# Kernel tuning notes

Hardware: AMD Instinct MI355X
Metric: run time of the kernel (lower is better)

The kernel has to match this reference:

```python
import math
import jax, jax.numpy as jnp
import numpy as np

D_MODEL = 1024
N_HEADS = 16
HEAD_DIM = D_MODEL // N_HEADS
ROPE_THETA = 10000.0


def setup_inputs() -> dict:
    key = jax.random.key(0)
    ks = jax.random.split(key, 5)
    B, T = 4, 2048
    # xavier-ish scale for weights
    w_scale = math.sqrt(2.0 / (D_MODEL + D_MODEL))
    return {
        "x": jax.random.normal(ks[0], (B, T, D_MODEL), dtype=jnp.float32),
        "Wq": jax.random.normal(ks[1], (D_MODEL, D_MODEL), dtype=jnp.float32) * w_scale,
        "Wk": jax.random.normal(ks[2], (D_MODEL, D_MODEL), dtype=jnp.float32) * w_scale,
        "Wv": jax.random.normal(ks[3], (D_MODEL, D_MODEL), dtype=jnp.float32) * w_scale,
        "Wo": jax.random.normal(ks[4], (D_MODEL, D_MODEL), dtype=jnp.float32) * w_scale,
    }


def _apply_rope(t, offset=0):
    # t: (B, H, T, Dh); standard half-rotation RoPE
    B, H, T, Dh = t.shape
    inv_freq = 1.0 / (ROPE_THETA ** (jnp.arange(0, Dh, 2, dtype=jnp.float32) / Dh))
    pos = jnp.arange(T, dtype=jnp.float32) + offset  # (T,)
    ang = pos[:, None] * inv_freq[None, :]           # (T, Dh/2)
    cos = jnp.concatenate([jnp.cos(ang), jnp.cos(ang)], axis=-1)  # (T, Dh)
    sin = jnp.concatenate([jnp.sin(ang), jnp.sin(ang)], axis=-1)
    t1, t2 = t[..., : Dh // 2], t[..., Dh // 2 :]
    rot = jnp.concatenate([-t2, t1], axis=-1)
    return t * cos + rot * sin


def _forward(x, Wq, Wk, Wv, Wo):
    B, T, _ = x.shape
    scale = 1.0 / math.sqrt(HEAD_DIM)

    def split_heads(y):  # (B,T,D) -> (B,H,T,Dh)
        return y.reshape(B, T, N_HEADS, HEAD_DIM).transpose(0, 2, 1, 3)

    q = split_heads(x @ Wq.T)
    k = split_heads(x @ Wk.T)
    v = split_heads(x @ Wv.T)

    q = _apply_rope(q)
    k = _apply_rope(k)

    # full materialized scores, as in the original manual SDPA
    scores = jnp.einsum("bhtd,bhsd->bhts", q, k) * scale  # (B,H,T,T)
    causal = jnp.triu(jnp.ones((T, T), dtype=bool), k=1)   # True = masked
    scores = jnp.where(causal[None, None], -jnp.inf, scores)
    attn = jax.nn.softmax(scores, axis=-1)
    attn = jnp.nan_to_num(attn, nan=0.0)
    out = jnp.einsum("bhts,bhsd->bhtd", attn, v)           # (B,H,T,Dh)
    out = out.transpose(0, 2, 1, 3).reshape(B, T, N_HEADS * HEAD_DIM)
    return out @ Wo.T


def reference(x, Wq, Wk, Wv, Wo):
    return _forward(x, Wq, Wk, Wv, Wo)
```

## Files before the change

kernel.cpp:

```cpp
#include <hip/hip_runtime.h>
#include <math.h>

typedef __bf16 bf16_t;
typedef __bf16 bf16x4 __attribute__((ext_vector_type(4)));
typedef __bf16 bf16x8 __attribute__((ext_vector_type(8)));
typedef float f32x4 __attribute__((ext_vector_type(4)));

#define MFMA16(a, b, c) __builtin_amdgcn_mfma_f32_16x16x32_bf16(a, b, c, 0, 0, 0)
#define GLD_LDS16(g, l)                                                                    \
    __builtin_amdgcn_global_load_lds((const __attribute__((address_space(1))) void*)(g),   \
                                     (__attribute__((address_space(3))) void*)(l), 16, 0, 0)

#define SM_SCALE_LOG2E 0.18033688011112042f
#define NEG_LOG2_10K_32 -0.41524101186092029f

#define SWZ(r, u) ((((r) << 6) + (u)) ^ ((((r) >> 1) & 7) << 4))

__device__ __forceinline__ void fast_sincos(float ang, float* s, float* c) {
    float rev = ang * 0.15915494309189535f;
    rev = rev - floorf(rev);
    *s = __builtin_amdgcn_sinf(rev);
    *c = __builtin_amdgcn_cosf(rev);
}

__global__ void cvt_all(const float* __restrict__ x, const float* __restrict__ wq,
                        const float* __restrict__ wk, const float* __restrict__ wv,
                        const float* __restrict__ wo, bf16_t* __restrict__ out) {
    long i = ((long)blockIdx.x * 256 + threadIdx.x) * 4;
    const float* src;
    long off;
    const long M1 = 1048576;
    if (i < 8 * M1) { src = x;  off = i; }
    else if (i < 9 * M1)  { src = wq; off = i - 8 * M1; }
    else if (i < 10 * M1) { src = wk; off = i - 9 * M1; }
    else if (i < 11 * M1) { src = wv; off = i - 10 * M1; }
    else                  { src = wo; off = i - 11 * M1; }
    float4 v = *(const float4*)(src + off);
    bf16x4 pk;
    pk[0] = (bf16_t)v.x;
    pk[1] = (bf16_t)v.y;
    pk[2] = (bf16_t)v.z;
    pk[3] = (bf16_t)v.w;
    *(bf16x4*)(out + i) = pk;
}

template <typename OutT>
__global__ __launch_bounds__(256) void gemm_bt(const bf16_t* __restrict__ A,
                                               const bf16_t* __restrict__ B,
                                               OutT* __restrict__ C,
                                               int M, int N, int K) {
    __shared__ __align__(16) bf16_t As[128 * 32];
    __shared__ __align__(16) bf16_t Bs[128 * 32];
    const int tid = threadIdx.x;
    const int lane = tid & 63, wave = tid >> 6;
    const int qd = lane >> 4, ln = lane & 15;
    int mt = blockIdx.y, nt = blockIdx.x;
    if ((gridDim.y & 7) == 0) {
        const int flat = blockIdx.x + gridDim.x * blockIdx.y;
        const int xcd = flat & 7, idx = flat >> 3;
        const int gy8 = gridDim.y >> 3;
        mt = xcd * gy8 + (idx % gy8);
        nt = idx / gy8;
    }
    const int m0 = mt * 128, n0 = nt * 128;
    const int wr = (wave >> 1) * 64, wc = (wave & 1) * 64;
    const int Kb = K * 2;

    f32x4 acc[4][4];
#pragma unroll
    for (int i = 0; i < 4; ++i)
#pragma unroll
        for (int j = 0; j < 4; ++j)
#pragma unroll
            for (int r = 0; r < 4; ++r) acc[i][j][r] = 0.f;

    const int off0 = wave * 2048 + lane * 16;
    const int off1 = off0 + 1024;
    const int r0 = off0 >> 6, c0 = off0 & 63;
    const int r1 = off1 >> 6, c1 = off1 & 63;

    for (int kt = 0; kt < K; kt += 32) {
        const char* Ab = (const char*)A + (size_t)m0 * Kb + kt * 2;
        const char* Bb = (const char*)B + (size_t)n0 * Kb + kt * 2;
        GLD_LDS16(Ab + (size_t)r0 * Kb + c0, (char*)As + wave * 2048);
        GLD_LDS16(Ab + (size_t)r1 * Kb + c1, (char*)As + wave * 2048 + 1024);
        GLD_LDS16(Bb + (size_t)r0 * Kb + c0, (char*)Bs + wave * 2048);
        GLD_LDS16(Bb + (size_t)r1 * Kb + c1, (char*)Bs + wave * 2048 + 1024);
        __syncthreads();
        bf16x8 af[4], bfr[4];
#pragma unroll
        for (int i = 0; i < 4; ++i)
            af[i] = *(const bf16x8*)(As + (wr + i * 16 + ln) * 32 + qd * 8);
#pragma unroll
        for (int j = 0; j < 4; ++j)
            bfr[j] = *(const bf16x8*)(Bs + (wc + j * 16 + ln) * 32 + qd * 8);
#pragma unroll
        for (int i = 0; i < 4; ++i)
#pragma unroll
            for (int j = 0; j < 4; ++j)
                acc[i][j] = MFMA16(af[i], bfr[j], acc[i][j]);
        __syncthreads();
    }
#pragma unroll
    for (int i = 0; i < 4; ++i)
#pragma unroll
        for (int j = 0; j < 4; ++j)
#pragma unroll
            for (int r = 0; r < 4; ++r) {
                int row = m0 + wr + i * 16 + qd * 4 + r;
                int col = n0 + wc + j * 16 + ln;
                C[(size_t)row * N + col] = (OutT)acc[i][j][r];
            }
}

__global__ __launch_bounds__(256) void gemm_qkv_rope8(const bf16_t* __restrict__ A,
                                                      const bf16_t* __restrict__ B,
                                                      bf16_t* __restrict__ Qo,
                                                      bf16_t* __restrict__ Ko,
                                                      bf16_t* __restrict__ Vt) {
    __shared__ __align__(16) bf16_t LA[2][2][128 * 32];
    __shared__ __align__(16) bf16_t LB[2][2][128 * 32];
    const int tid = threadIdx.x;
    const int wave = tid >> 6, lane = tid & 63;
    const int qd = lane >> 4, ln = lane & 15;
    const int wrr = wave >> 1, wcc = wave & 1;
    const int m0 = blockIdx.y * 128, n0 = blockIdx.x * 128;

    f32x4 acc[4][4];
#pragma unroll
    for (int m = 0; m < 4; ++m)
#pragma unroll
        for (int n = 0; n < 4; ++n)
#pragma unroll
            for (int r = 0; r < 4; ++r) acc[m][n][r] = 0.f;

    const int soff = wave * 1024 + lane * 16;
    const int slog = soff ^ (((soff >> 7) & 7) << 4);
    const int srow = slog >> 6;
    const int scol = slog & 63;
    const char* Abase = (const char*)A + (size_t)(m0 + srow) * 2048 + scol;
    const char* Bbase = (const char*)B + (size_t)(n0 + srow) * 2048 + scol;

    int aoff[4], boff[4];
#pragma unroll
    for (int m = 0; m < 4; ++m) {
        int r = wrr * 64 + m * 16 + ln;
        aoff[m] = ((r << 6) + (qd << 4)) ^ (((r >> 1) & 7) << 4);
    }
#pragma unroll
    for (int n = 0; n < 4; ++n) {
        int r = wcc * 64 + n * 16 + ln;
        boff[n] = ((r << 6) + (qd << 4)) ^ (((r >> 1) & 7) << 4);
    }

    auto stageA = [&](int kt, int kh, int nb) {
        const char* g = Abase + kt * 128 + kh * 64;
        char* l = (char*)&LA[nb][kh][0] + wave * 1024;
        GLD_LDS16(g, l);
        GLD_LDS16(g + (size_t)64 * 2048, l + 4096);
    };
    auto stageB = [&](int kt, int kh, int nb) {
        const char* g = Bbase + kt * 128 + kh * 64;
        char* l = (char*)&LB[nb][kh][0] + wave * 1024;
        GLD_LDS16(g, l);
        GLD_LDS16(g + (size_t)64 * 2048, l + 4096);
    };

    bf16x8 fA[4], fB[4];
#define LOAD_B(kh, bb_)                                          \
    {                                                            \
        const char* base_ = (const char*)&LB[bb_][kh][0];        \
        fB[0] = *(const bf16x8*)(base_ + boff[0]);               \
        fB[1] = *(const bf16x8*)(base_ + boff[1]);               \
        fB[2] = *(const bf16x8*)(base_ + boff[2]);               \
        fB[3] = *(const bf16x8*)(base_ + boff[3]);               \
    }
#define LOAD_A(kh, bb_)                                          \
    {                                                            \
        const char* base_ = (const char*)&LA[bb_][kh][0];        \
        fA[0] = *(const bf16x8*)(base_ + aoff[0]);               \
        fA[1] = *(const bf16x8*)(base_ + aoff[1]);               \
        fA[2] = *(const bf16x8*)(base_ + aoff[2]);               \
        fA[3] = *(const bf16x8*)(base_ + aoff[3]);               \
    }
#define MFMA_Q()                                                                 \
    {                                                                            \
        __builtin_amdgcn_s_setprio(1);                                           \
        _Pragma("unroll") for (int mm = 0; mm < 4; ++mm)                         \
            _Pragma("unroll") for (int nn = 0; nn < 4; ++nn)                     \
                acc[mm][nn] = MFMA16(fA[mm], fB[nn], acc[mm][nn]);               \
        __builtin_amdgcn_s_setprio(0);                                           \
    }
#define BAR __builtin_amdgcn_s_barrier()
#define WAIT_LGKM asm volatile("s_waitcnt lgkmcnt(0)" ::: "memory")
#define VMCNT4 asm volatile("s_waitcnt vmcnt(4)" ::: "memory")
#define VMCNT0 asm volatile("s_waitcnt vmcnt(0)" ::: "memory")

    stageB(0, 0, 0);
    stageA(0, 0, 0);
    stageB(0, 1, 0);
    stageA(0, 1, 0);
    VMCNT4;
    BAR;

    int buf = 0;
    for (int kt = 0; kt < 16; ++kt) {
        const int nb = buf ^ 1;
        const bool pre = (kt + 1 < 16);
        LOAD_B(0, buf);
        LOAD_A(0, buf);
        if (pre) { stageB(kt + 1, 0, nb); stageA(kt + 1, 0, nb); }
        BAR;
        WAIT_LGKM;
        MFMA_Q();
        if (pre) { VMCNT4; } else { VMCNT0; }
        BAR;
        LOAD_B(1, buf);
        LOAD_A(1, buf);
        if (pre) { stageB(kt + 1, 1, nb); stageA(kt + 1, 1, nb); }
        BAR;
        WAIT_LGKM;
        MFMA_Q();
        if (pre) { VMCNT4; } else { VMCNT0; }
        BAR;
        buf = nb;
    }
#undef LOAD_B
#undef LOAD_A
#undef MFMA_Q
#undef BAR
#undef WAIT_LGKM
#undef VMCNT4
#undef VMCNT0

    if (n0 < 2048) {
        const bool isQ = (n0 < 1024);
        bf16_t* Out = isQ ? Qo : Ko;
        const float scale = isQ ? SM_SCALE_LOG2E : 1.0f;
        const int nc0 = (n0 & 1023) + wcc * 64;
        const float inv0 = exp2f((float)ln * NEG_LOG2_10K_32);
        const float inv1 = exp2f((float)(ln + 16) * NEG_LOG2_10K_32);
#pragma unroll
        for (int m = 0; m < 4; ++m) {
#pragma unroll
            for (int r = 0; r < 4; ++r) {
                int row = m0 + wrr * 64 + m * 16 + qd * 4 + r;
                int t = row & 2047, bb = row >> 11;
                float ft = (float)t;
                float s0, c0v, s1, c1v;
                fast_sincos(ft * inv0, &s0, &c0v);
                fast_sincos(ft * inv1, &s1, &c1v);
#pragma unroll
                for (int n = 0; n < 4; ++n) {
                    int col = nc0 + n * 16 + ln;
                    int h = col >> 6, d = col & 63;
                    float sv = (n & 1) ? s1 : s0;
                    float cv = (n & 1) ? c1v : c0v;
                    float td = acc[m][n][r], tp = acc[m][n ^ 2][r];
                    float o = (n < 2) ? (td * cv - tp * sv) : (td * cv + tp * sv);
                    Out[((size_t)(bb * 16 + h) * 2048 + t) * 64 + d] = (bf16_t)(o * scale);
                }
            }
        }
    } else {
        const int nv0 = (n0 - 2048) + wcc * 64;
#pragma unroll
        for (int m = 0; m < 4; ++m) {
            int tb = m0 + wrr * 64 + m * 16 + qd * 4;
            int t = tb & 2047, bb = tb >> 11;
#pragma unroll
            for (int n = 0; n < 4; ++n) {
                int col = nv0 + n * 16 + ln;
                int h = col >> 6, d = col & 63;
                bf16x4 pk;
#pragma unroll
                for (int r = 0; r < 4; ++r) pk[r] = (bf16_t)acc[m][n][r];
                *(bf16x4*)(Vt + ((size_t)(bb * 16 + h) * 64 + d) * 2048 + t) = pk;
            }
        }
    }
}

__global__ __launch_bounds__(256) void attn_fwd(const bf16_t* __restrict__ Qg,
                                                const bf16_t* __restrict__ Kg,
                                                const bf16_t* __restrict__ Vtg,
                                                bf16_t* __restrict__ Og) {
    __shared__ __align__(16) bf16_t Kt[2 * 64 * 32];
    __shared__ __align__(16) bf16_t Vl[2 * 64 * 32];
    __shared__ __align__(16) bf16_t Pl[4][2 * 32 * 32];
    const int id = blockIdx.x;
    const int bh = ((id & 7) << 3) | ((id >> 3) & 7);
    const int pair = (id >> 6) & 7;
    const int b = bh >> 4, h = bh & 15;
    const int tid = threadIdx.x, wave = tid >> 6, lane = tid & 63;
    const int qd = lane >> 4, ln = lane & 15;
    const int kr0r = tid >> 3, kr1r = 32 + (tid >> 3);
    const int ch = tid & 7;
    const int kr0c = ch * 8;
    const int wh = (ch >> 2) * 4096;
    const int wu = (ch & 3) << 4;
    const int wo0 = wh + SWZ(kr0r, wu);
    const int wo1 = wh + SWZ(kr1r, wu);
    const bf16_t* Kbh = Kg + (size_t)bh * 2048 * 64;
    const bf16_t* Vbh = Vtg + (size_t)bh * 64 * 2048;

    bf16x8 vones;
#pragma unroll
    for (int i = 0; i < 8; ++i) vones[i] = (bf16_t)1.0f;

    for (int ph = 0; ph < 2; ++ph) {
        const int qt = ph ? 15 - pair : pair;
        const int q0 = qt * 128;
        const int wrow = q0 + wave * 32;
        const int njt = 2 * qt + 2;

        bf16x8 aq[2][2];
#pragma unroll
        for (int f = 0; f < 2; ++f) {
            const bf16_t* Qbase = Qg + ((size_t)bh * 2048 + wrow + f * 16 + ln) * 64;
            aq[f][0] = *(const bf16x8*)(Qbase + qd * 8);
            aq[f][1] = *(const bf16x8*)(Qbase + 32 + qd * 8);
        }

        f32x4 lsum[2];
        f32x4 o_acc[2][4];
#pragma unroll
        for (int f = 0; f < 2; ++f) {
#pragma unroll
            for (int r = 0; r < 4; ++r) lsum[f][r] = 0.f;
#pragma unroll
            for (int c = 0; c < 4; ++c)
#pragma unroll
                for (int r = 0; r < 4; ++r) o_acc[f][c][r] = 0.f;
        }

        int4 kr0, kr1, vr0, vr1;
        auto issue = [&](int j) {
            const bf16_t* kp = Kbh + (size_t)j * 64 * 64;
            const bf16_t* vp = Vbh + j * 64;
            kr0 = *(const int4*)(kp + kr0r * 64 + kr0c);
            kr1 = *(const int4*)(kp + kr1r * 64 + kr0c);
            vr0 = *(const int4*)(vp + (size_t)kr0r * 2048 + kr0c);
            vr1 = *(const int4*)(vp + (size_t)kr1r * 2048 + kr0c);
        };
        issue(0);

        for (int j = 0; j < njt; ++j) {
            __syncthreads();
            *(int4*)((char*)Kt + wo0) = kr0;
            *(int4*)((char*)Kt + wo1) = kr1;
            *(int4*)((char*)Vl + wo0) = vr0;
            *(int4*)((char*)Vl + wo1) = vr1;
            __syncthreads();
            if (j + 1 < njt) issue(j + 1);

            if (j * 64 > wrow + 31) continue;
            const int j64 = j * 64;

            f32x4 s[2][4];
            __builtin_amdgcn_s_setprio(1);
#pragma unroll
            for (int st = 0; st < 4; ++st) {
                const int rk = st * 16 + ln;
                bf16x8 bk0 = *(const bf16x8*)((const char*)Kt + SWZ(rk, qd * 16));
                bf16x8 bk1 = *(const bf16x8*)((const char*)Kt + 4096 + SWZ(rk, qd * 16));
#pragma unroll
                for (int f = 0; f < 2; ++f) {
                    f32x4 t = {0.f, 0.f, 0.f, 0.f};
                    t = MFMA16(aq[f][0], bk0, t);
                    t = MFMA16(aq[f][1], bk1, t);
                    s[f][st] = t;
                }
            }
            __builtin_amdgcn_s_setprio(0);

            if (j64 + 63 <= wrow) {
#pragma unroll
                for (int f = 0; f < 2; ++f)
#pragma unroll
                    for (int st = 0; st < 4; ++st)
#pragma unroll
                        for (int r = 0; r < 4; ++r)
                            s[f][st][r] = __builtin_amdgcn_exp2f(s[f][st][r]);
            } else {
#pragma unroll
                for (int f = 0; f < 2; ++f) {
                    int rowb = wrow + f * 16 + qd * 4;
#pragma unroll
                    for (int st = 0; st < 4; ++st) {
                        int col = j64 + st * 16 + ln;
#pragma unroll
                        for (int r = 0; r < 4; ++r) {
                            float v = (col > rowb + r) ? -INFINITY : s[f][st][r];
                            s[f][st][r] = __builtin_amdgcn_exp2f(v);
                        }
                    }
                }
            }

            char* Pw = (char*)&Pl[wave][0];
#pragma unroll
            for (int f = 0; f < 2; ++f)
#pragma unroll
                for (int st = 0; st < 4; ++st) {
                    const int ph2 = (st >> 1) * 2048;
                    const int pu = ((st & 1) * 16 + ln) * 2;
#pragma unroll
                    for (int r = 0; r < 4; ++r) {
                        const int prow = f * 16 + qd * 4 + r;
                        *(bf16_t*)(Pw + ph2 + SWZ(prow, pu)) = (bf16_t)s[f][st][r];
                    }
                }

            bf16x8 bv[4][2];
#pragma unroll
            for (int ct = 0; ct < 4; ++ct) {
                const int rv = ct * 16 + ln;
                bv[ct][0] = *(const bf16x8*)((const char*)Vl + SWZ(rv, qd * 16));
                bv[ct][1] = *(const bf16x8*)((const char*)Vl + 4096 + SWZ(rv, qd * 16));
            }
            __builtin_amdgcn_s_setprio(1);
#pragma unroll
            for (int f = 0; f < 2; ++f) {
                const int rp = f * 16 + ln;
                bf16x8 ap0 = *(const bf16x8*)(Pw + SWZ(rp, qd * 16));
                bf16x8 ap1 = *(const bf16x8*)(Pw + 2048 + SWZ(rp, qd * 16));
                lsum[f] = MFMA16(ap0, vones, lsum[f]);
                lsum[f] = MFMA16(ap1, vones, lsum[f]);
#pragma unroll
                for (int ct = 0; ct < 4; ++ct) {
                    o_acc[f][ct] = MFMA16(ap0, bv[ct][0], o_acc[f][ct]);
                    o_acc[f][ct] = MFMA16(ap1, bv[ct][1], o_acc[f][ct]);
                }
            }
            __builtin_amdgcn_s_setprio(0);
        }

#pragma unroll
        for (int f = 0; f < 2; ++f) {
            size_t obase = ((size_t)b * 2048 + wrow + f * 16 + qd * 4) * 1024 + h * 64;
            float rl[4];
#pragma unroll
            for (int r = 0; r < 4; ++r) rl[r] = __builtin_amdgcn_rcpf(lsum[f][r]);
#pragma unroll
            for (int ct = 0; ct < 4; ++ct)
#pragma unroll
                for (int r = 0; r < 4; ++r)
                    Og[obase + (size_t)r * 1024 + ct * 16 + ln] =
                        (bf16_t)(o_acc[f][ct][r] * rl[r]);
        }
    }
}

extern "C" void kernel_launch(void* const* d_in, const int* in_sizes, int n_in,
                              void* d_out, int out_size, void* d_ws, size_t ws_size,
                              hipStream_t stream) {
    (void)in_sizes; (void)n_in; (void)out_size; (void)ws_size;
    const float* x  = (const float*)d_in[0];
    const float* Wq = (const float*)d_in[1];
    const float* Wk = (const float*)d_in[2];
    const float* Wv = (const float*)d_in[3];
    const float* Wo = (const float*)d_in[4];
    char* ws = (char*)d_ws;
    const size_t MB = 1ull << 20;
    bf16_t* xb   = (bf16_t*)(ws + 0);
    bf16_t* wqb  = (bf16_t*)(ws + 16 * MB);
    bf16_t* wob  = (bf16_t*)(ws + 22 * MB);
    bf16_t* Qb   = (bf16_t*)(ws + 24 * MB);
    bf16_t* Kb   = (bf16_t*)(ws + 40 * MB);
    bf16_t* Vtb  = (bf16_t*)(ws + 56 * MB);
    bf16_t* AOb  = xb;

    cvt_all<<<dim3(12288), dim3(256), 0, stream>>>(x, Wq, Wk, Wv, Wo, (bf16_t*)ws);

    gemm_qkv_rope8<<<dim3(24, 64), dim3(256), 0, stream>>>(xb, wqb, Qb, Kb, Vtb);

    attn_fwd<<<dim3(512), dim3(256), 0, stream>>>(Qb, Kb, Vtb, AOb);

    gemm_bt<float><<<dim3(8, 64), dim3(256), 0, stream>>>(AOb, wob, (float*)d_out, 8192, 1024, 1024);
}
```

Baseline: 254.2 us.

## Double-buffer output projection GEMM with swizzled LDS and async prefetch

Rewrites the output-projection GEMM as a specialized fixed-shape kernel. It uses double-buffered LDS with the next K tile prefetched through global_load_lds while MFMAs run on the current tile. LDS is XOR-swizzled to cut bank conflicts, and scheduling uses explicit waitcnt, barriers and setprio. This hides global-load latency that the old single-buffered loop, with its two syncs per step, exposed. In exchange it uses more LDS per block, which may lower occupancy, and it hardcodes M/N/K.

```diff
diff --git a/kernel.cpp b/kernel.cpp
--- a/kernel.cpp
+++ b/kernel.cpp
@@ -44,72 +44,136 @@
     *(bf16x4*)(out + i) = pk;
 }
 
-template <typename OutT>
 __global__ __launch_bounds__(256) void gemm_bt(const bf16_t* __restrict__ A,
                                                const bf16_t* __restrict__ B,
-                                               OutT* __restrict__ C,
-                                               int M, int N, int K) {
-    __shared__ __align__(16) bf16_t As[128 * 32];
-    __shared__ __align__(16) bf16_t Bs[128 * 32];
+                                               float* __restrict__ C) {
+    __shared__ __align__(16) bf16_t LA[2][2][128 * 32];
+    __shared__ __align__(16) bf16_t LB[2][2][128 * 32];
     const int tid = threadIdx.x;
-    const int lane = tid & 63, wave = tid >> 6;
+    const int wave = tid >> 6, lane = tid & 63;
     const int qd = lane >> 4, ln = lane & 15;
-    int mt = blockIdx.y, nt = blockIdx.x;
-    if ((gridDim.y & 7) == 0) {
-        const int flat = blockIdx.x + gridDim.x * blockIdx.y;
-        const int xcd = flat & 7, idx = flat >> 3;
-        const int gy8 = gridDim.y >> 3;
-        mt = xcd * gy8 + (idx % gy8);
-        nt = idx / gy8;
-    }
+    const int wrr = wave >> 1, wcc = wave & 1;
+    const int flat = blockIdx.x + gridDim.x * blockIdx.y;
+    const int xcd = flat & 7, idx = flat >> 3;
+    const int mt = xcd * 8 + (idx & 7), nt = idx >> 3;
     const int m0 = mt * 128, n0 = nt * 128;
-    const int wr = (wave >> 1) * 64, wc = (wave & 1) * 64;
-    const int Kb = K * 2;
 
     f32x4 acc[4][4];
 #pragma unroll
-    for (int i = 0; i < 4; ++i)
-#pragma unroll
-        for (int j = 0; j < 4; ++j)
-#pragma unroll
-            for (int r = 0; r < 4; ++r) acc[i][j][r] = 0.f;
-
-    const int off0 = wave * 2048 + lane * 16;
-    const int off1 = off0 + 1024;
-    const int r0 = off0 >> 6, c0 = off0 & 63;
-    const int r1 = off1 >> 6, c1 = off1 & 63;
-
-    for (int kt = 0; kt < K; kt += 32) {
-        const char* Ab = (const char*)A + (size_t)m0 * Kb + kt * 2;
-        const char* Bb = (const char*)B + (size_t)n0 * Kb + kt * 2;
-        GLD_LDS16(Ab + (size_t)r0 * Kb + c0, (char*)As + wave * 2048);
-        GLD_LDS16(Ab + (size_t)r1 * Kb + c1, (char*)As + wave * 2048 + 1024);
-        GLD_LDS16(Bb + (size_t)r0 * Kb + c0, (char*)Bs + wave * 2048);
-        GLD_LDS16(Bb + (size_t)r1 * Kb + c1, (char*)Bs + wave * 2048 + 1024);
-        __syncthreads();
-        bf16x8 af[4], bfr[4];
-#pragma unroll
-        for (int i = 0; i < 4; ++i)
-            af[i] = *(const bf16x8*)(As + (wr + i * 16 + ln) * 32 + qd * 8);
-#pragma unroll
-        for (int j = 0; j < 4; ++j)
-            bfr[j] = *(const bf16x8*)(Bs + (wc + j * 16 + ln) * 32 + qd * 8);
-#pragma unroll
-        for (int i = 0; i < 4; ++i)
-#pragma unroll
-            for (int j = 0; j < 4; ++j)
-                acc[i][j] = MFMA16(af[i], bfr[j], acc[i][j]);
-        __syncthreads();
-    }
-#pragma unroll
-    for (int i = 0; i < 4; ++i)
-#pragma unroll
-        for (int j = 0; j < 4; ++j)
+    for (int m = 0; m < 4; ++m)
+#pragma unroll
+        for (int n = 0; n < 4; ++n)
+#pragma unroll
+            for (int r = 0; r < 4; ++r) acc[m][n][r] = 0.f;
+
+    const int soff = wave * 1024 + lane * 16;
+    const int slog = soff ^ (((soff >> 7) & 7) << 4);
+    const int srow = slog >> 6;
+    const int scol = slog & 63;
+    const char* Abase = (const char*)A + (size_t)(m0 + srow) * 2048 + scol;
+    const char* Bbase = (const char*)B + (size_t)(n0 + srow) * 2048 + scol;
+
+    int aoff[4], boff[4];
+#pragma unroll
+    for (int m = 0; m < 4; ++m) {
+        int r = wrr * 64 + m * 16 + ln;
+        aoff[m] = ((r << 6) + (qd << 4)) ^ (((r >> 1) & 7) << 4);
+    }
+#pragma unroll
+    for (int n = 0; n < 4; ++n) {
+        int r = wcc * 64 + n * 16 + ln;
+        boff[n] = ((r << 6) + (qd << 4)) ^ (((r >> 1) & 7) << 4);
+    }
+
+    auto stageA = [&](int kt, int kh, int nb) {
+        const char* g = Abase + kt * 128 + kh * 64;
+        char* l = (char*)&LA[nb][kh][0] + wave * 1024;
+        GLD_LDS16(g, l);
+        GLD_LDS16(g + (size_t)64 * 2048, l + 4096);
+    };
+    auto stageB = [&](int kt, int kh, int nb) {
+        const char* g = Bbase + kt * 128 + kh * 64;
+        char* l = (char*)&LB[nb][kh][0] + wave * 1024;
+        GLD_LDS16(g, l);
+        GLD_LDS16(g + (size_t)64 * 2048, l + 4096);
+    };
+
+    bf16x8 fA[4], fB[4];
+#define LOAD_B(kh, bb_)                                          \
+    {                                                            \
+        const char* base_ = (const char*)&LB[bb_][kh][0];        \
+        fB[0] = *(const bf16x8*)(base_ + boff[0]);               \
+        fB[1] = *(const bf16x8*)(base_ + boff[1]);               \
+        fB[2] = *(const bf16x8*)(base_ + boff[2]);               \
+        fB[3] = *(const bf16x8*)(base_ + boff[3]);               \
+    }
+#define LOAD_A(kh, bb_)                                          \
+    {                                                            \
+        const char* base_ = (const char*)&LA[bb_][kh][0];        \
+        fA[0] = *(const bf16x8*)(base_ + aoff[0]);               \
+        fA[1] = *(const bf16x8*)(base_ + aoff[1]);               \
+        fA[2] = *(const bf16x8*)(base_ + aoff[2]);               \
+        fA[3] = *(const bf16x8*)(base_ + aoff[3]);               \
+    }
+#define MFMA_Q()                                                                 \
+    {                                                                            \
+        __builtin_amdgcn_s_setprio(1);                                           \
+        _Pragma("unroll") for (int mm = 0; mm < 4; ++mm)                         \
+            _Pragma("unroll") for (int nn = 0; nn < 4; ++nn)                     \
+                acc[mm][nn] = MFMA16(fA[mm], fB[nn], acc[mm][nn]);               \
+        __builtin_amdgcn_s_setprio(0);                                           \
+    }
+#define BAR __builtin_amdgcn_s_barrier()
+#define WAIT_LGKM asm volatile("s_waitcnt lgkmcnt(0)" ::: "memory")
+#define VMCNT4 asm volatile("s_waitcnt vmcnt(4)" ::: "memory")
+#define VMCNT0 asm volatile("s_waitcnt vmcnt(0)" ::: "memory")
+
+    stageB(0, 0, 0);
+    stageA(0, 0, 0);
+    stageB(0, 1, 0);
+    stageA(0, 1, 0);
+    VMCNT4;
+    BAR;
+
+    int buf = 0;
+    for (int kt = 0; kt < 16; ++kt) {
+        const int nb = buf ^ 1;
+        const bool pre = (kt + 1 < 16);
+        LOAD_B(0, buf);
+        LOAD_A(0, buf);
+        if (pre) { stageB(kt + 1, 0, nb); stageA(kt + 1, 0, nb); }
+        BAR;
+        WAIT_LGKM;
+        MFMA_Q();
+        if (pre) { VMCNT4; } else { VMCNT0; }
+        BAR;
+        LOAD_B(1, buf);
+        LOAD_A(1, buf);
+        if (pre) { stageB(kt + 1, 1, nb); stageA(kt + 1, 1, nb); }
+        BAR;
+        WAIT_LGKM;
+        MFMA_Q();
+        if (pre) { VMCNT4; } else { VMCNT0; }
+        BAR;
+        buf = nb;
+    }
+#undef LOAD_B
+#undef LOAD_A
+#undef MFMA_Q
+#undef BAR
+#undef WAIT_LGKM
+#undef VMCNT4
+#undef VMCNT0
+
+#pragma unroll
+    for (int m = 0; m < 4; ++m)
+#pragma unroll
+        for (int n = 0; n < 4; ++n)
 #pragma unroll
             for (int r = 0; r < 4; ++r) {
-                int row = m0 + wr + i * 16 + qd * 4 + r;
-                int col = n0 + wc + j * 16 + ln;
-                C[(size_t)row * N + col] = (OutT)acc[i][j][r];
+                int row = m0 + wrr * 64 + m * 16 + qd * 4 + r;
+                int col = n0 + wcc * 64 + n * 16 + ln;
+                C[(size_t)row * 1024 + col] = acc[m][n][r];
             }
 }
 
@@ -477,5 +541,5 @@
 
     attn_fwd<<<dim3(512), dim3(256), 0, stream>>>(Qb, Kb, Vtb, AOb);
 
-    gemm_bt<float><<<dim3(8, 64), dim3(256), 0, stream>>>(AOb, wob, (float*)d_out, 8192, 1024, 1024);
+    gemm_bt<<<dim3(8, 64), dim3(256), 0, stream>>>(AOb, wob, (float*)d_out);
 }
```

Result: faster. 247.6 us (-2.6%).
